# Kernel optimization log

Measured on AMD Instinct MI355X. Metric: run time of the kernel, lower is better.

Reference implementation:

```python
import jax, jax.numpy as jnp
import numpy as np

N, IN, HID, OUT, HD = 512, 256, 256, 256, 64  # n_agents, in_dim, hid_dim, out_dim, head_dim (out_dim // n_heads)


def _mlp2(x, w1, b1, w2, b2):
    return jax.nn.relu(x @ w1.T + b1) @ w2.T + b2


def setup_inputs():
    key = jax.random.key(0)
    ks = jax.random.split(key, 32)
    p = lambda i, shape: jax.random.normal(ks[i], shape, dtype=jnp.float32) * 0.05
    V = jax.random.normal(ks[0], (N, IN), dtype=jnp.float32)
    adj = jax.random.randint(ks[1], (N, N), 0, 2, dtype=jnp.int32)
    adj = adj.at[jnp.arange(N), jnp.arange(N)].set(1)  # self-loops so no softmax row is all -inf
    prev_hidden = jax.random.normal(ks[2], (N, HID), dtype=jnp.float32)
    return {
        "V": V, "adj": adj, "prev_hidden": prev_hidden,
        "W1": p(3, (HID, IN)), "sa0": p(4, (HID,)), "sa1": p(5, (HID,)),
        "ce_w1": p(6, (HID, 2 * IN)), "ce_b1": p(7, (HID,)), "ce_w2": p(8, (HD, HID)), "ce_b2": p(9, (HD,)),
        "ca0": p(10, (HD,)), "ca1": p(11, (HD,)),
        "te_w1": p(12, (HID, IN + HID)), "te_b1": p(13, (HID,)), "te_w2": p(14, (HD, HID)), "te_b2": p(15, (HD,)),
        "ta0": p(16, (HD,)), "ta1": p(17, (HD,)),
        "pe_w1": p(18, (HID, 3 * IN)), "pe_b1": p(19, (HID,)), "pe_w2": p(20, (HD, HID)), "pe_b2": p(21, (HD,)),
        "pa0": p(22, (HD,)), "pa1": p(23, (HD,)),
        "W2": p(24, (OUT, HID + 2 * HD + 1)), "op_w": p(25, (OUT, OUT)), "op_b": p(26, (OUT,)),
        "ln_g": jnp.ones((OUT,), jnp.float32), "ln_b": jnp.zeros((OUT,), jnp.float32),
    }


def _forward(V, adj, prev_hidden, W1, sa0, sa1, ce_w1, ce_b1, ce_w2, ce_b2, ca0, ca1,
             te_w1, te_b1, te_w2, te_b2, ta0, ta1, pe_w1, pe_b1, pe_w2, pe_b2, pa0, pa1,
             W2, op_w, op_b, ln_g, ln_b):
    neg = -jnp.inf
    # --- branch 1: standard GAT attention ---
    Wh1 = V @ W1.T                                             # (N, HID)
    s1 = (Wh1 @ sa0)[:, None] + (Wh1 @ sa1)[None, :]           # (N, N)
    s1 = jnp.where(adj == 0, neg, s1)
    H1 = jax.nn.softmax(s1, axis=1) @ Wh1                      # (N, HID)
    # --- branch 2: causal, all ordered pairs i != j ---
    wA, wB = ce_w1[:, :IN], ce_w1[:, IN:]
    h = jax.nn.relu((V @ wA.T)[:, None, :] + (V @ wB.T)[None, :, :] + ce_b1)  # (N, N, HID)
    f = h @ ce_w2.T + ce_b2                                    # (N, N, HD)
    s2 = jnp.where(jnp.eye(N, dtype=bool), neg, f @ (ca0 + ca1))
    a2 = jax.nn.softmax(s2.reshape(-1)).reshape(N, N)          # softmax over all off-diagonal pairs
    H2 = jnp.broadcast_to(jnp.einsum('ij,ijd->d', a2, f), (N, HD))
    # --- branch 3: temporal; (N,1) scores broadcast against (N,N) causal mask ---
    tf = _mlp2(jnp.concatenate([V, prev_hidden], -1), te_w1, te_b1, te_w2, te_b2)  # (N, HD)
    ts = tf @ (ta0 + ta1)                                      # (N,)
    cmask = jnp.triu(jnp.ones((N, N), dtype=bool), 1)
    s3 = jnp.where(cmask, neg, jnp.broadcast_to(ts[:, None], (N, N)))
    H3 = jax.nn.softmax(s3, axis=1) @ tf                       # (N, HD) == prefix means of tf
    # --- branch 4: cooperative; first two neighbors in index order (zeros if < 2) ---
    pos = jnp.where(adj == 1, jnp.arange(N)[None, :], N)
    srt = jnp.sort(pos, axis=1)
    i0, i1 = srt[:, 0], srt[:, 1]
    valid = (i1 < N)[:, None]
    n0 = jnp.where(valid, V[jnp.clip(i0, 0, N - 1)], 0.0)
    n1 = jnp.where(valid, V[jnp.clip(i1, 0, N - 1)], 0.0)
    cf = _mlp2(jnp.concatenate([V, n0, n1], -1), pe_w1, pe_b1, pe_w2, pe_b2)  # (N, HD)
    # torch: softmax over dim of size 1 -> all ones, alpha^T @ cf == column sums -> (HD,)
    # then unsqueezed to (HD,1) and zero-padded to (N,1) since HD < N  (faithful to source bug)
    H4v = cf.sum(axis=0)
    H4 = jnp.concatenate([H4v, jnp.zeros((N - HD,), V.dtype)])[:, None]       # (N, 1)
    # --- combine ---
    Hc = jnp.concatenate([H1, H2, H3, H4], axis=-1) @ W2.T     # (N, OUT)
    out = Hc @ op_w.T + op_b
    mu = out.mean(-1, keepdims=True)
    var = ((out - mu) ** 2).mean(-1, keepdims=True)
    y = (out - mu) / jnp.sqrt(var + 1e-5) * ln_g + ln_b        # LayerNorm, eps=1e-5
    return jax.nn.elu(y)                                       # dropout is identity in eval


def reference(V, adj, prev_hidden, W1, sa0, sa1, ce_w1, ce_b1, ce_w2, ce_b2, ca0, ca1,
              te_w1, te_b1, te_w2, te_b2, ta0, ta1, pe_w1, pe_b1, pe_w2, pe_b2, pa0, pa1,
              W2, op_w, op_b, ln_g, ln_b):
    return _forward(V, adj, prev_hidden, W1, sa0, sa1, ce_w1, ce_b1, ce_w2, ce_b2, ca0, ca1,
                    te_w1, te_b1, te_w2, te_b2, ta0, ta1, pe_w1, pe_b1, pe_w2, pe_b2, pa0, pa1,
                    W2, op_w, op_b, ln_g, ln_b)
```

## Files before the change

### kernel.cpp

```cpp
#include <hip/hip_runtime.h>

typedef unsigned short u16;

constexpr int kN   = 512;
constexpr int kIN  = 256;
constexpr int kHID = 256;
constexpr int kHD  = 64;
constexpr int kOUT = 256;

__device__ __forceinline__ float us2f(u16 u){
  union { unsigned int i; float f; } c; c.i = ((unsigned int)u) << 16; return c.f;
}
__device__ __forceinline__ u16 f2us(float f){
  union { float f; unsigned int i; } c; c.f = f;
  unsigned int r = c.i + 0x7fff + ((c.i >> 16) & 1);
  return (u16)(r >> 16);
}

__device__ bool probe_is_f32(const unsigned int* __restrict__ V){
  __shared__ int cnt;
  if (threadIdx.x == 0) cnt = 0;
  __syncthreads();
  int c = 0;
  for (int k = threadIdx.x; k < 4096; k += 256){
    float x = us2f((u16)(V[k] & 0xffffu));
    if (!(fabsf(x) <= 32.0f)) c++;
  }
  atomicAdd(&cnt, c);
  __syncthreads();
  return cnt > 64;
}

struct ConvArgs { const void* src[23]; float* dst[23]; int n[23]; };

__global__ __launch_bounds__(256) void k_conv(ConvArgs a, const unsigned int* __restrict__ Vraw,
                                              const int* __restrict__ adj, int* __restrict__ flag,
                                              float* __restrict__ Xp, float* __restrict__ e1v)
{
  int b = blockIdx.x, tid = threadIdx.x;
  bool f32 = probe_is_f32(Vraw);
  if (b < 256){
    if (b == 0){
      if (tid == 0) *flag = f32 ? 1 : 0;
      e1v[tid] = 0.f; e1v[tid + 256] = 0.f;
    }
    int t = b*256 + tid;
    const int stride = 65536;
    for (int s = 0; s < 23; ++s){
      int n4 = a.n[s] >> 2;
      float4* d = (float4*)a.dst[s];
      if (f32){
        const float4* sf = (const float4*)a.src[s];
        for (int i = t; i < n4; i += stride) d[i] = sf[i];
      } else {
        const ushort4* sb = (const ushort4*)a.src[s];
        for (int i = t; i < n4; i += stride){
          ushort4 u = sb[i];
          d[i] = make_float4(us2f(u.x), us2f(u.y), us2f(u.z), us2f(u.w));
        }
      }
    }
  } else {
    __shared__ unsigned long long msk[8];
    __shared__ int sj[2];
    int i = b - 256;
    int w = tid >> 6, lane = tid & 63;
    unsigned long long m0 = __ballot(adj[(size_t)i*kN + tid] != 0);
    unsigned long long m1 = __ballot(adj[(size_t)i*kN + 256 + tid] != 0);
    if (lane == 0){ msk[w] = m0; msk[4 + w] = m1; }
    __syncthreads();
    if (tid == 0){
      int j0 = -1, j1 = -1;
      for (int c = 0; c < 8 && j1 < 0; ++c){
        unsigned long long m = msk[c];
        while (m && j1 < 0){
          int bb = __builtin_ctzll(m);
          int j = c*64 + bb;
          if (j0 < 0) j0 = j; else j1 = j;
          m &= m - 1;
        }
      }
      if (j1 < 0) j0 = -1;
      sj[0] = j0; sj[1] = j1;
    }
    __syncthreads();
    int j0 = sj[0], j1 = sj[1];
    const float* Vf = (const float*)Vraw;
    const u16*  Vb = (const u16*)Vraw;
    auto rdV = [&](int r, int k)->float{
      return f32 ? Vf[(size_t)r*kIN + k] : us2f(Vb[(size_t)r*kIN + k]);
    };
    Xp[(size_t)i*768 + tid]       = rdV(i, tid);
    Xp[(size_t)i*768 + 256 + tid] = (j0 >= 0) ? rdV(j0, tid) : 0.f;
    Xp[(size_t)i*768 + 512 + tid] = (j1 >= 0) ? rdV(j1, tid) : 0.f;
  }
}

__device__ __forceinline__ float blk_red(float v, float* tmp, bool isMax){
  int lane = threadIdx.x & 63, wv = threadIdx.x >> 6;
  #pragma unroll
  for (int o = 32; o > 0; o >>= 1){
    float t = __shfl_down(v, o, 64);
    v = isMax ? fmaxf(v, t) : (v + t);
  }
  __syncthreads();
  if (lane == 0) tmp[wv] = v;
  __syncthreads();
  float r = tmp[0];
  for (int i = 1; i < 4; ++i) r = isMax ? fmaxf(r, tmp[i]) : (r + tmp[i]);
  return r;
}

struct WSP {
  const int* adj; const int* flag; void* out;
  float *Vf,*prevf,*W1f,*sa1f,*cw1f,*cb1f,*cw2f,*cb2f,*ca0f,*ca1f;
  float *tw1f,*tb1f,*tw2f,*tb2f,*pw1f,*pb1f,*pw2f,*pb2f;
  float *W2f,*opwf,*opbf,*lngf,*lnbf;
  float *tw2t,*pw2t,*Wcomb,*OM,*ow4;
  float *Wh1,*e1v,*wadj,*Hc,*Am,*Bm,*uvec,*beta;
  float *s2,*maxp,*zp,*MZ,*gsum;
  float *htp0,*htp1,*hpp0,*hpp1,*hpp2,*hidden_t,*hidden_p;
  float *tfm,*cfm,*H4v,*Xp,*out3;
};

struct GSeg2 { const float* X; const float* W; float* C; int ldx, ldw, ldc, K; };
struct GArgs2 { GSeg2 s[8]; const float* sa1; float* e1; };

__global__ __launch_bounds__(256) void k_gemmA(GArgs2 ga)
{
  __shared__ __align__(16) float Xs[2][32][68];
  __shared__ __align__(16) float Ws[2][32][68];
  const GSeg2 sg = ga.s[blockIdx.y];
  const int tm = blockIdx.x & 7;
  const int tn = blockIdx.x >> 3;
  const int i0 = tm << 6;
  const int n0 = tn << 6;
  const int tid = threadIdx.x;

  const int xrow = tid >> 3;
  const int xk   = (tid & 7) << 2;
  const int rg = (tid >> 4) << 2;
  const int cg = (tid & 15) << 2;

  const float* Xb = sg.X + (size_t)i0 * sg.ldx;
  const float* Wb = sg.W + (size_t)n0 * sg.ldw;

  float4 xr0, xr1, wr0, wr1;
  auto loadT = [&](int kt){
    xr0 = *(const float4*)(Xb + (size_t)xrow * sg.ldx + kt + xk);
    xr1 = *(const float4*)(Xb + (size_t)(xrow+32) * sg.ldx + kt + xk);
    wr0 = *(const float4*)(Wb + (size_t)xrow * sg.ldw + kt + xk);
    wr1 = *(const float4*)(Wb + (size_t)(xrow+32) * sg.ldw + kt + xk);
  };
  auto writeT = [&](int bu){
    Xs[bu][xk+0][xrow] = xr0.x;  Xs[bu][xk+1][xrow] = xr0.y;
    Xs[bu][xk+2][xrow] = xr0.z;  Xs[bu][xk+3][xrow] = xr0.w;
    Xs[bu][xk+0][xrow+32] = xr1.x;  Xs[bu][xk+1][xrow+32] = xr1.y;
    Xs[bu][xk+2][xrow+32] = xr1.z;  Xs[bu][xk+3][xrow+32] = xr1.w;
    Ws[bu][xk+0][xrow]    = wr0.x; Ws[bu][xk+1][xrow]    = wr0.y;
    Ws[bu][xk+2][xrow]    = wr0.z; Ws[bu][xk+3][xrow]    = wr0.w;
    Ws[bu][xk+0][xrow+32] = wr1.x; Ws[bu][xk+1][xrow+32] = wr1.y;
    Ws[bu][xk+2][xrow+32] = wr1.z; Ws[bu][xk+3][xrow+32] = wr1.w;
  };

  loadT(0); writeT(0); __syncthreads();

  float acc[4][4] = {};
  const int nkt = sg.K >> 5;
  for (int t = 0; t < nkt; ++t){
    if (t + 1 < nkt) loadT((t + 1) << 5);
    const int bu = t & 1;
    #pragma unroll
    for (int kk = 0; kk < 32; ++kk){
      const float4 av = *(const float4*)&Xs[bu][kk][rg];
      const float4 bv = *(const float4*)&Ws[bu][kk][cg];
      acc[0][0]+=av.x*bv.x; acc[0][1]+=av.x*bv.y; acc[0][2]+=av.x*bv.z; acc[0][3]+=av.x*bv.w;
      acc[1][0]+=av.y*bv.x; acc[1][1]+=av.y*bv.y; acc[1][2]+=av.y*bv.z; acc[1][3]+=av.y*bv.w;
      acc[2][0]+=av.z*bv.x; acc[2][1]+=av.z*bv.y; acc[2][2]+=av.z*bv.z; acc[2][3]+=av.z*bv.w;
      acc[3][0]+=av.w*bv.x; acc[3][1]+=av.w*bv.y; acc[3][2]+=av.w*bv.z; acc[3][3]+=av.w*bv.w;
    }
    if (t + 1 < nkt) writeT((t + 1) & 1);
    __syncthreads();
  }

  #pragma unroll
  for (int ri = 0; ri < 4; ++ri)
    *(float4*)(sg.C + (size_t)(i0 + rg + ri) * sg.ldc + (n0 + cg)) =
      make_float4(acc[ri][0], acc[ri][1], acc[ri][2], acc[ri][3]);

  if (blockIdx.y == 0){
    int cb = n0 + cg;
    float s0 = ga.sa1[cb], s1 = ga.sa1[cb+1], s2v = ga.sa1[cb+2], s3 = ga.sa1[cb+3];
    #pragma unroll
    for (int ri = 0; ri < 4; ++ri){
      float v = acc[ri][0]*s0 + acc[ri][1]*s1 + acc[ri][2]*s2v + acc[ri][3]*s3;
      v += __shfl_xor(v, 1, 16);
      v += __shfl_xor(v, 2, 16);
      v += __shfl_xor(v, 4, 16);
      v += __shfl_xor(v, 8, 16);
      if ((tid & 15) == 0) atomicAdd(&ga.e1[i0 + rg + ri], v);
    }
  }
}

struct GS32 { const float* X; const float* W; float* C; int ldx, ldw, ldc, K; int bkn; };

__device__ __forceinline__ void gemm32_body(const GS32 sg, int tm, int tn, int tid,
                                            float* Xs, float* Ws)
{
  const int i0 = tm << 5, n0 = tn << 5;
  const int xrow = tid >> 3;
  const int xk = (tid & 7) << 2;
  const int rg = (tid >> 4) << 1;
  const int cg = (tid & 15) << 1;
  const float* Xb = sg.X + (size_t)i0 * sg.ldx;
  const float* Wb = sg.bkn ? (sg.W + n0) : (sg.W + (size_t)n0 * sg.ldw);
  float4 xr, wr;
  auto loadT = [&](int kt){
    xr = *(const float4*)(Xb + (size_t)xrow * sg.ldx + kt + xk);
    if (sg.bkn) wr = *(const float4*)(Wb + (size_t)(kt + xrow) * sg.ldw + xk);
    else        wr = *(const float4*)(Wb + (size_t)xrow * sg.ldw + kt + xk);
  };
  auto writeT = [&](int bu){
    float* xs = Xs + bu*1152;
    xs[(xk+0)*36 + xrow] = xr.x; xs[(xk+1)*36 + xrow] = xr.y;
    xs[(xk+2)*36 + xrow] = xr.z; xs[(xk+3)*36 + xrow] = xr.w;
    float* wsp = Ws + bu*1152;
    if (sg.bkn){
      wsp[xrow*36 + xk+0] = wr.x; wsp[xrow*36 + xk+1] = wr.y;
      wsp[xrow*36 + xk+2] = wr.z; wsp[xrow*36 + xk+3] = wr.w;
    } else {
      wsp[(xk+0)*36 + xrow] = wr.x; wsp[(xk+1)*36 + xrow] = wr.y;
      wsp[(xk+2)*36 + xrow] = wr.z; wsp[(xk+3)*36 + xrow] = wr.w;
    }
  };
  loadT(0); writeT(0); __syncthreads();
  float a00=0,a01=0,a10=0,a11=0;
  const int nkt = sg.K >> 5;
  for (int t = 0; t < nkt; ++t){
    if (t+1 < nkt) loadT((t+1) << 5);
    const float* xs = Xs + (t&1)*1152;
    const float* wsp = Ws + (t&1)*1152;
    #pragma unroll
    for (int kk = 0; kk < 32; ++kk){
      float2 av = *(const float2*)&xs[kk*36 + rg];
      float2 bv = *(const float2*)&wsp[kk*36 + cg];
      a00 += av.x*bv.x; a01 += av.x*bv.y;
      a10 += av.y*bv.x; a11 += av.y*bv.y;
    }
    if (t+1 < nkt) writeT((t+1)&1);
    __syncthreads();
  }
  float* cp = sg.C + (size_t)(i0+rg)*sg.ldc + n0 + cg;
  *(float2*)cp = make_float2(a00, a01);
  *(float2*)(cp + sg.ldc) = make_float2(a10, a11);
}

__global__ __launch_bounds__(256) void k_stage2(WSP w)
{
  __shared__ __align__(16) char smem[18432];
  float* st = (float*)smem;
  int b = blockIdx.x, tid = threadIdx.x;
  if (b < 128){
    int f = b*256 + tid;
    int c4 = f & 63;
    {
      float4 a = ((const float4*)w.htp0)[f], bb = ((const float4*)w.htp1)[f];
      float4 bi = ((const float4*)w.tb1f)[c4];
      ((float4*)w.hidden_t)[f] = make_float4(
        fmaxf(a.x+bb.x+bi.x,0.f), fmaxf(a.y+bb.y+bi.y,0.f),
        fmaxf(a.z+bb.z+bi.z,0.f), fmaxf(a.w+bb.w+bi.w,0.f));
    }
    {
      float4 a = ((const float4*)w.hpp0)[f], bb = ((const float4*)w.hpp1)[f];
      float4 c = ((const float4*)w.hpp2)[f];
      float4 bi = ((const float4*)w.pb1f)[c4];
      ((float4*)w.hidden_p)[f] = make_float4(
        fmaxf(a.x+bb.x+c.x+bi.x,0.f), fmaxf(a.y+bb.y+c.y+bi.y,0.f),
        fmaxf(a.z+bb.z+c.z+bi.z,0.f), fmaxf(a.w+bb.w+c.w+bi.w,0.f));
    }
  } else if (b < 640){
    int i = b - 128;
    int m0 = w.adj[(size_t)i*kN + tid];
    int m1 = w.adj[(size_t)i*kN + tid + 256];
    float ea = w.e1v[tid], eb = w.e1v[tid+256];
    float v0 = m0 ? ea : -1e30f;
    float v1 = m1 ? eb : -1e30f;
    float m = blk_red(fmaxf(v0, v1), st, true);
    float z = blk_red((m0 ? expf(ea-m) : 0.f) + (m1 ? expf(eb-m) : 0.f), st, false);
    float iz = 1.0f / z;
    w.wadj[(size_t)i*kN + tid]       = m0 ? expf(ea - m) * iz : 0.f;
    w.wadj[(size_t)i*kN + tid + 256] = m1 ? expf(eb - m) * iz : 0.f;
  } else if (b == 640){
    if (tid < 64){ st[tid] = w.ca0f[tid] + w.ca1f[tid]; w.H4v[tid] = 0.f; }
    __syncthreads();
    float a = 0.f;
    for (int d = 0; d < kHD; ++d) a += w.cw2f[(size_t)d*kHID + tid] * st[d];
    w.uvec[tid] = a;
    if (tid == 0){
      float bsum = 0.f;
      for (int d = 0; d < kHD; ++d) bsum += w.cb2f[d] * st[d];
      *w.beta = bsum;
    }
  } else if (b < 643){
    const float* src = (b == 641) ? w.tw2f : w.pw2f;
    float* dst = (b == 641) ? w.tw2t : w.pw2t;
    for (int ch = 0; ch < 4; ++ch){
      __syncthreads();
      #pragma unroll
      for (int e = 0; e < 16; ++e){
        int lin = e*256 + tid;
        int r = lin >> 6, c = lin & 63;
        st[r*65 + c] = src[(size_t)r*256 + ch*64 + c];
      }
      __syncthreads();
      #pragma unroll
      for (int e = 0; e < 16; ++e){
        int lin = e*256 + tid;
        int kc = lin >> 6, dd = lin & 63;
        dst[(size_t)(ch*64 + kc)*64 + dd] = st[dd*65 + kc];
      }
    }
  } else if (b < 723){
    int q = b - 643;
    int tm = q & 7, tn = q >> 3;
    const float* Wsrc = w.W2f + ((tn < 8) ? 0 : 64);
    GS32 sg{w.opwf, Wsrc, w.Wcomb, 256, 385, 320, 256, 1};
    gemm32_body(sg, tm, tn, tid, (float*)smem, (float*)(smem + 9216));
  } else if (b < 739){
    int q = b - 723;
    GS32 sg{w.opwf, w.W2f + 256, w.OM, 256, 385, 64, 256, 1};
    gemm32_body(sg, q & 7, q >> 3, tid, (float*)smem, (float*)(smem + 9216));
  } else {
    st[tid] = w.W2f[(size_t)tid*385 + 384];
    __syncthreads();
    float a = 0.f;
    const float* orow = w.opwf + (size_t)tid*256;
    for (int m = 0; m < 256; m += 4){
      float4 o4 = *(const float4*)(orow + m);
      a += o4.x*st[m] + o4.y*st[m+1] + o4.z*st[m+2] + o4.w*st[m+3];
    }
    w.ow4[tid] = a;
  }
}

__global__ __launch_bounds__(256) void k_stage3(WSP w)
{
  __shared__ __align__(16) float smem3[4*256 + 256];
  int b = blockIdx.x, tid = threadIdx.x;
  if (b < 64){
    int m = b >> 5, grp = b & 31;
    const float* X  = m ? w.hidden_p : w.hidden_t;
    const float* Wt = m ? w.pw2t : w.tw2t;
    const float* bi = m ? w.pb2f : w.tb2f;
    float* C = m ? w.cfm : w.tfm;
    int i0 = grp*16 + (tid >> 6)*4;
    int d = tid & 63;
    const float* x0 = X + (size_t)i0*256;
    const float* x1 = x0 + 256;
    const float* x2 = x0 + 512;
    const float* x3 = x0 + 768;
    float a0=0.f, a1=0.f, a2=0.f, a3=0.f;
    for (int k = 0; k < 256; k += 4){
      float w0 = Wt[(size_t)(k+0)*64 + d];
      float w1 = Wt[(size_t)(k+1)*64 + d];
      float w2 = Wt[(size_t)(k+2)*64 + d];
      float w3 = Wt[(size_t)(k+3)*64 + d];
      float4 f0 = *(const float4*)(x0 + k);
      float4 f1 = *(const float4*)(x1 + k);
      float4 f2 = *(const float4*)(x2 + k);
      float4 f3 = *(const float4*)(x3 + k);
      a0 += f0.x*w0 + f0.y*w1 + f0.z*w2 + f0.w*w3;
      a1 += f1.x*w0 + f1.y*w1 + f1.z*w2 + f1.w*w3;
      a2 += f2.x*w0 + f2.y*w1 + f2.z*w2 + f2.w*w3;
      a3 += f3.x*w0 + f3.y*w1 + f3.z*w2 + f3.w*w3;
    }
    float bd = bi[d];
    C[(size_t)(i0+0)*64 + d] = a0 + bd;
    C[(size_t)(i0+1)*64 + d] = a1 + bd;
    C[(size_t)(i0+2)*64 + d] = a2 + bd;
    C[(size_t)(i0+3)*64 + d] = a3 + bd;
  } else {
    float* aib = smem3;
    float* uu  = smem3 + 1024;
    int q = b - 64;
    int i0 = (q & 127) * 4, j0 = (q >> 7) * 64;
    int wv = tid >> 6, lane = tid & 63;
    uu[tid] = w.uvec[tid];
    float b1v = w.cb1f[tid];
    #pragma unroll
    for (int r = 0; r < 4; ++r) aib[r*256 + tid] = w.Am[(size_t)(i0+r)*kHID + tid] + b1v;
    __syncthreads();
    int i = i0 + wv, j = j0 + lane;
    const float4* bp = (const float4*)(w.Bm + (size_t)j*kHID);
    float acc = *w.beta;
    #pragma unroll 8
    for (int k4 = 0; k4 < kHID/4; ++k4){
      float4 bv = bp[k4];
      float4 a4 = *(const float4*)&aib[wv*256 + k4*4];
      float4 u4 = *(const float4*)&uu[k4*4];
      acc += fmaxf(a4.x+bv.x,0.f)*u4.x + fmaxf(a4.y+bv.y,0.f)*u4.y
           + fmaxf(a4.z+bv.z,0.f)*u4.z + fmaxf(a4.w+bv.w,0.f)*u4.w;
    }
    if (j == i) acc = -1e30f;
    w.s2[(size_t)i*kN + j] = acc;
    float m = acc;
    #pragma unroll
    for (int o = 32; o > 0; o >>= 1) m = fmaxf(m, __shfl_down(m, o, 64));
    m = __shfl(m, 0, 64);
    float e = expf(acc - m);
    #pragma unroll
    for (int o = 32; o > 0; o >>= 1) e += __shfl_down(e, o, 64);
    if (lane == 0){
      int pb = q*4 + wv;
      w.maxp[pb] = m; w.zp[pb] = e;
    }
  }
}

__global__ __launch_bounds__(256) void k_stage4(WSP w)
{
  __shared__ __align__(16) char smem[18432];
  int b = blockIdx.x, tid = threadIdx.x;
  if (b < 128){
    GS32 sg{w.wadj, w.Wh1, w.Hc, 512, 256, 320, 512, 1};
    gemm32_body(sg, b & 15, b >> 4, tid, (float*)smem, (float*)(smem + 9216));
  } else if (b < 192){
    int d = b - 128;
    int lane = tid & 63, wv = tid >> 6;
    float v0 = w.tfm[(size_t)(2*tid)*kHD + d];
    float v1 = w.tfm[(size_t)(2*tid+1)*kHD + d];
    float s = v0 + v1;
    float x = s;
    #pragma unroll
    for (int off = 1; off < 64; off <<= 1){
      float y = __shfl_up(x, off, 64);
      if (lane >= off) x += y;
    }
    float* wsum = (float*)smem;
    if (lane == 63) wsum[wv] = x;
    __syncthreads();
    float base = 0.f;
    for (int k = 0; k < wv; ++k) base += wsum[k];
    float excl = base + x - s;
    w.Hc[(size_t)(2*tid)*320 + 256 + d]   = (excl + v0) / (float)(2*tid + 1);
    w.Hc[(size_t)(2*tid+1)*320 + 256 + d] = (excl + s)  / (float)(2*tid + 2);
  } else if (b < 200){
    float* sm = (float*)smem;
    int d = tid & 63, sub = tid >> 6;
    int r0 = (b-192)*64 + sub*16;
    float s = 0.f;
    #pragma unroll
    for (int e = 0; e < 16; ++e) s += w.cfm[(size_t)(r0+e)*kHD + d];
    sm[sub*64 + d] = s;
    __syncthreads();
    if (tid < 64)
      atomicAdd(&w.H4v[tid], sm[tid] + sm[64+tid] + sm[128+tid] + sm[192+tid]);
  } else {
    float* red = (float*)smem;
    float m = -1e30f;
    #pragma unroll
    for (int r = 0; r < 16; ++r) m = fmaxf(m, w.maxp[tid + 256*r]);
    m = blk_red(m, red, true);
    float z = 0.f;
    #pragma unroll
    for (int r = 0; r < 16; ++r) z += w.zp[tid + 256*r] * expf(w.maxp[tid + 256*r] - m);
    z = blk_red(z, red, false);
    if (tid == 0){ w.MZ[0] = m; w.MZ[1] = z; }
    w.gsum[tid] = 0.f;
  }
}

__global__ __launch_bounds__(256) void k_stage5(WSP w)
{
  __shared__ __align__(16) char smem[18432];
  int b = blockIdx.x, tid = threadIdx.x;
  if (b < 1024){
    float* wt = (float*)smem;
    int i0 = (b & 31) * 16, j0 = (b >> 5) * 16;
    float M = w.MZ[0], invZ = 1.0f / w.MZ[1];
    {
      int r = tid >> 4, c = tid & 15;
      wt[r*16 + c] = expf(w.s2[(size_t)(i0+r)*kN + (j0+c)] - M) * invZ;
    }
    float b1v = w.cb1f[tid];
    float aib[16];
    #pragma unroll
    for (int r = 0; r < 16; ++r) aib[r] = w.Am[(size_t)(i0+r)*kHID + tid] + b1v;
    __syncthreads();
    float acc = 0.f;
    for (int j = 0; j < 16; ++j){
      float bj = w.Bm[(size_t)(j0+j)*kHID + tid];
      #pragma unroll
      for (int r = 0; r < 16; ++r)
        acc += wt[r*16 + j] * fmaxf(aib[r] + bj, 0.f);
    }
    atomicAdd(&w.gsum[tid], acc);
  } else {
    int q = b - 1024;
    GS32 sg{w.Hc, w.Wcomb, w.out3, 320, 320, 256, 320, 0};
    gemm32_body(sg, q & 15, q >> 4, tid, (float*)smem, (float*)(smem + 9216));
  }
}

__global__ __launch_bounds__(256) void k_final(WSP w)
{
  __shared__ float gs[kHID];
  __shared__ float part[kHD][4];
  __shared__ float h2s[kHD];
  __shared__ float cc2s[kOUT];
  int b = blockIdx.x, tid = threadIdx.x;
  gs[tid] = w.gsum[tid];
  __syncthreads();
  {
    int dd = tid >> 2, q = tid & 3;
    float a = 0.f;
    for (int kk = 0; kk < 64; ++kk){
      int k = q*64 + kk;
      a += gs[k] * w.cw2f[(size_t)dd*kHID + k];
    }
    part[dd][q] = a;
  }
  __syncthreads();
  if (tid < kHD)
    h2s[tid] = w.cb2f[tid] + part[tid][0] + part[tid][1] + part[tid][2] + part[tid][3];
  __syncthreads();
  {
    float a = 0.f;
    const float* om = w.OM + (size_t)tid*64;
    for (int d = 0; d < kHD; d += 4){
      float4 o4 = *(const float4*)(om + d);
      a += o4.x*h2s[d] + o4.y*h2s[d+1] + o4.z*h2s[d+2] + o4.w*h2s[d+3];
    }
    cc2s[tid] = a;
  }
  __syncthreads();
  int row = b*4 + (tid >> 6), lane = tid & 63;
  float h4r = (row < kHD) ? w.H4v[row] : 0.f;
  float4 v  = *(const float4*)(w.out3 + (size_t)row*kOUT + lane*4);
  float4 c2 = *(const float4*)(&cc2s[lane*4]);
  float4 o4 = *(const float4*)(w.ow4 + lane*4);
  float4 pb = *(const float4*)(w.opbf + lane*4);
  v.x += c2.x + h4r*o4.x + pb.x;
  v.y += c2.y + h4r*o4.y + pb.y;
  v.z += c2.z + h4r*o4.z + pb.z;
  v.w += c2.w + h4r*o4.w + pb.w;
  float s = v.x + v.y + v.z + v.w;
  #pragma unroll
  for (int o = 32; o > 0; o >>= 1) s += __shfl_xor(s, o, 64);
  float mu = s * (1.0f/kOUT);
  float dx = v.x-mu, dy = v.y-mu, dz = v.z-mu, dw = v.w-mu;
  float ss = dx*dx + dy*dy + dz*dz + dw*dw;
  #pragma unroll
  for (int o = 32; o > 0; o >>= 1) ss += __shfl_xor(ss, o, 64);
  float rs = rsqrtf(ss * (1.0f/kOUT) + 1e-5f);
  float4 g  = *(const float4*)(w.lngf + lane*4);
  float4 be = *(const float4*)(w.lnbf + lane*4);
  float y0 = dx*rs*g.x + be.x, y1 = dy*rs*g.y + be.y;
  float y2 = dz*rs*g.z + be.z, y3 = dw*rs*g.w + be.w;
  y0 = (y0 > 0.f) ? y0 : expm1f(y0);
  y1 = (y1 > 0.f) ? y1 : expm1f(y1);
  y2 = (y2 > 0.f) ? y2 : expm1f(y2);
  y3 = (y3 > 0.f) ? y3 : expm1f(y3);
  if (*w.flag){
    *(float4*)((float*)w.out + (size_t)row*kOUT + lane*4) = make_float4(y0,y1,y2,y3);
  } else {
    ushort4 u; u.x = f2us(y0); u.y = f2us(y1); u.z = f2us(y2); u.w = f2us(y3);
    ((ushort4*)w.out)[(size_t)row*64 + lane] = u;
  }
}

extern "C" void kernel_launch(void* const* d_in, const int* in_sizes, int n_in,
                              void* d_out, int out_size, void* d_ws, size_t ws_size,
                              hipStream_t stream)
{
  const void* V     = d_in[0];
  const int*  adj   = (const int*)d_in[1];
  const void* prev  = d_in[2];
  const void* W1    = d_in[3];
  const void* sa1   = d_in[5];
  const void* ce_w1 = d_in[6];
  const void* ce_b1 = d_in[7];
  const void* ce_w2 = d_in[8];
  const void* ce_b2 = d_in[9];
  const void* ca0   = d_in[10];
  const void* ca1   = d_in[11];
  const void* te_w1 = d_in[12];
  const void* te_b1 = d_in[13];
  const void* te_w2 = d_in[14];
  const void* te_b2 = d_in[15];
  const void* pe_w1 = d_in[18];
  const void* pe_b1 = d_in[19];
  const void* pe_w2 = d_in[20];
  const void* pe_b2 = d_in[21];
  const void* W2    = d_in[24];
  const void* op_w  = d_in[25];
  const void* op_b  = d_in[26];
  const void* ln_g  = d_in[27];
  const void* ln_b  = d_in[28];

  float* ws  = (float*)d_ws;
  int*  flag = (int*)ws;
  float* p   = ws + 16;
  float* Vf   = p; p += 131072;
  float* prevf= p; p += 131072;
  float* W1f  = p; p += 65536;
  float* sa1f = p; p += 256;
  float* cw1f = p; p += 131072;
  float* cb1f = p; p += 256;
  float* cw2f = p; p += 16384;
  float* cb2f = p; p += 64;
  float* ca0f = p; p += 64;
  float* ca1f = p; p += 64;
  float* tw1f = p; p += 131072;
  float* tb1f = p; p += 256;
  float* tw2f = p; p += 16384;
  float* tb2f = p; p += 64;
  float* pw1f = p; p += 196608;
  float* pb1f = p; p += 256;
  float* pw2f = p; p += 16384;
  float* pb2f = p; p += 64;
  float* W2f  = p; p += 98560;
  float* opwf = p; p += 65536;
  float* opbf = p; p += 256;
  float* lngf = p; p += 256;
  float* lnbf = p; p += 256;
  float* tw2t = p; p += 16384;
  float* pw2t = p; p += 16384;
  float* Wcomb= p; p += 81920;
  float* OM   = p; p += 16384;
  float* ow4  = p; p += 256;
  float* Wh1      = p; p += 131072;
  float* e1v      = p; p += 512;
  float* wadj     = p; p += 262144;
  float* Hc       = p; p += 163840;
  float* Am       = p; p += 131072;
  float* Bm       = p; p += 131072;
  float* uvec     = p; p += 256;
  float* beta     = p; p += 16;
  float* s2       = p; p += 262144;
  float* maxp     = p; p += 4096;
  float* zpart    = p; p += 4096;
  float* MZ       = p; p += 16;
  float* gsum     = p; p += 256;
  float* htp0     = p; p += 131072;
  float* htp1     = p; p += 131072;
  float* hpp0     = p; p += 131072;
  float* hpp1     = p; p += 131072;
  float* hpp2     = p; p += 131072;
  float* hidden_t = p; p += 131072;
  float* hidden_p = p; p += 131072;
  float* tfm      = p; p += 32768;
  float* cfm      = p; p += 32768;
  float* H4v      = p; p += 64;
  float* Xp       = p; p += 393216;
  float* out3     = p; p += 131072;

  WSP w;
  w.adj = adj; w.flag = flag; w.out = d_out;
  w.Vf=Vf; w.prevf=prevf; w.W1f=W1f; w.sa1f=sa1f; w.cw1f=cw1f; w.cb1f=cb1f;
  w.cw2f=cw2f; w.cb2f=cb2f; w.ca0f=ca0f; w.ca1f=ca1f;
  w.tw1f=tw1f; w.tb1f=tb1f; w.tw2f=tw2f; w.tb2f=tb2f;
  w.pw1f=pw1f; w.pb1f=pb1f; w.pw2f=pw2f; w.pb2f=pb2f;
  w.W2f=W2f; w.opwf=opwf; w.opbf=opbf; w.lngf=lngf; w.lnbf=lnbf;
  w.tw2t=tw2t; w.pw2t=pw2t; w.Wcomb=Wcomb; w.OM=OM; w.ow4=ow4;
  w.Wh1=Wh1; w.e1v=e1v; w.wadj=wadj; w.Hc=Hc;
  w.Am=Am; w.Bm=Bm; w.uvec=uvec; w.beta=beta;
  w.s2=s2; w.maxp=maxp; w.zp=zpart; w.MZ=MZ; w.gsum=gsum;
  w.htp0=htp0; w.htp1=htp1; w.hpp0=hpp0; w.hpp1=hpp1; w.hpp2=hpp2;
  w.hidden_t=hidden_t; w.hidden_p=hidden_p;
  w.tfm=tfm; w.cfm=cfm; w.H4v=H4v; w.Xp=Xp; w.out3=out3;

  {
    ConvArgs ca;
    const void* srcs[23] = {V, prev, W1, sa1, ce_w1, ce_b1, ce_w2, ce_b2, ca0, ca1,
                            te_w1, te_b1, te_w2, te_b2, pe_w1, pe_b1, pe_w2, pe_b2,
                            W2, op_w, op_b, ln_g, ln_b};
    float* dsts[23] = {Vf, prevf, W1f, sa1f, cw1f, cb1f, cw2f, cb2f, ca0f, ca1f,
                       tw1f, tb1f, tw2f, tb2f, pw1f, pb1f, pw2f, pb2f,
                       W2f, opwf, opbf, lngf, lnbf};
    int ns[23] = {131072, 131072, 65536, 256, 131072, 256, 16384, 64, 64, 64,
                  131072, 256, 16384, 64, 196608, 256, 16384, 64,
                  98560, 65536, 256, 256, 256};
    for (int s = 0; s < 23; ++s){ ca.src[s] = srcs[s]; ca.dst[s] = dsts[s]; ca.n[s] = ns[s]; }
    k_conv<<<768, 256, 0, stream>>>(ca, (const unsigned int*)V, adj, flag, Xp, e1v);
  }

  {
    GArgs2 g{};
    g.s[0] = {Vf,       W1f,        Wh1,  256, 256, 256, 256};
    g.s[1] = {Vf,       cw1f,       Am,   256, 512, 256, 256};
    g.s[2] = {Vf,       cw1f + 256, Bm,   256, 512, 256, 256};
    g.s[3] = {Vf,       tw1f,       htp0, 256, 512, 256, 256};
    g.s[4] = {prevf,    tw1f + 256, htp1, 256, 512, 256, 256};
    g.s[5] = {Xp,       pw1f,       hpp0, 768, 768, 256, 256};
    g.s[6] = {Xp + 256, pw1f + 256, hpp1, 768, 768, 256, 256};
    g.s[7] = {Xp + 512, pw1f + 512, hpp2, 768, 768, 256, 256};
    g.sa1 = sa1f; g.e1 = e1v;
    k_gemmA<<<dim3(32, 8), 256, 0, stream>>>(g);
  }

  k_stage2<<<740, 256, 0, stream>>>(w);

  k_stage3<<<1088, 256, 0, stream>>>(w);

  k_stage4<<<201, 256, 0, stream>>>(w);

  k_stage5<<<1152, 256, 0, stream>>>(w);

  k_final<<<128, 256, 0, stream>>>(w);
}
```

Before: 243.0 us.

## Fuse all stages into one cooperative persistent kernel with grid syncs

Replaces seven separate kernel launches with a single cooperative persistent kernel that loops over stages and separates them with grid-wide barriers. Stage work is repacked, so some independent pieces (weight transposes, the uvec/beta reduction, the W2/op_w combination GEMMs) move earlier and read raw inputs directly. The goal is to remove launch gaps and tail effects between stages. In exchange it adds grid.sync cost, a larger per-block shared-memory footprint that may limit occupancy, and a fallback path of per-stage launches.

```diff
diff --git a/kernel.cpp b/kernel.cpp
--- a/kernel.cpp
+++ b/kernel.cpp
@@ -1,4 +1,7 @@
 #include <hip/hip_runtime.h>
+#include <hip/hip_cooperative_groups.h>
+
+namespace cg = cooperative_groups;
 
 typedef unsigned short u16;
 
@@ -15,6 +18,9 @@
   union { float f; unsigned int i; } c; c.f = f;
   unsigned int r = c.i + 0x7fff + ((c.i >> 16) & 1);
   return (u16)(r >> 16);
+}
+__device__ __forceinline__ float ldraw(const void* p, size_t i, bool f32){
+  return f32 ? ((const float*)p)[i] : us2f(((const u16*)p)[i]);
 }
 
 __device__ bool probe_is_f32(const unsigned int* __restrict__ V){
@@ -31,71 +37,6 @@
   return cnt > 64;
 }
 
-struct ConvArgs { const void* src[23]; float* dst[23]; int n[23]; };
-
-__global__ __launch_bounds__(256) void k_conv(ConvArgs a, const unsigned int* __restrict__ Vraw,
-                                              const int* __restrict__ adj, int* __restrict__ flag,
-                                              float* __restrict__ Xp, float* __restrict__ e1v)
-{
-  int b = blockIdx.x, tid = threadIdx.x;
-  bool f32 = probe_is_f32(Vraw);
-  if (b < 256){
-    if (b == 0){
-      if (tid == 0) *flag = f32 ? 1 : 0;
-      e1v[tid] = 0.f; e1v[tid + 256] = 0.f;
-    }
-    int t = b*256 + tid;
-    const int stride = 65536;
-    for (int s = 0; s < 23; ++s){
-      int n4 = a.n[s] >> 2;
-      float4* d = (float4*)a.dst[s];
-      if (f32){
-        const float4* sf = (const float4*)a.src[s];
-        for (int i = t; i < n4; i += stride) d[i] = sf[i];
-      } else {
-        const ushort4* sb = (const ushort4*)a.src[s];
-        for (int i = t; i < n4; i += stride){
-          ushort4 u = sb[i];
-          d[i] = make_float4(us2f(u.x), us2f(u.y), us2f(u.z), us2f(u.w));
-        }
-      }
-    }
-  } else {
-    __shared__ unsigned long long msk[8];
-    __shared__ int sj[2];
-    int i = b - 256;
-    int w = tid >> 6, lane = tid & 63;
-    unsigned long long m0 = __ballot(adj[(size_t)i*kN + tid] != 0);
-    unsigned long long m1 = __ballot(adj[(size_t)i*kN + 256 + tid] != 0);
-    if (lane == 0){ msk[w] = m0; msk[4 + w] = m1; }
-    __syncthreads();
-    if (tid == 0){
-      int j0 = -1, j1 = -1;
-      for (int c = 0; c < 8 && j1 < 0; ++c){
-        unsigned long long m = msk[c];
-        while (m && j1 < 0){
-          int bb = __builtin_ctzll(m);
-          int j = c*64 + bb;
-          if (j0 < 0) j0 = j; else j1 = j;
-          m &= m - 1;
-        }
-      }
-      if (j1 < 0) j0 = -1;
-      sj[0] = j0; sj[1] = j1;
-    }
-    __syncthreads();
-    int j0 = sj[0], j1 = sj[1];
-    const float* Vf = (const float*)Vraw;
-    const u16*  Vb = (const u16*)Vraw;
-    auto rdV = [&](int r, int k)->float{
-      return f32 ? Vf[(size_t)r*kIN + k] : us2f(Vb[(size_t)r*kIN + k]);
-    };
-    Xp[(size_t)i*768 + tid]       = rdV(i, tid);
-    Xp[(size_t)i*768 + 256 + tid] = (j0 >= 0) ? rdV(j0, tid) : 0.f;
-    Xp[(size_t)i*768 + 512 + tid] = (j1 >= 0) ? rdV(j1, tid) : 0.f;
-  }
-}
-
 __device__ __forceinline__ float blk_red(float v, float* tmp, bool isMax){
   int lane = threadIdx.x & 63, wv = threadIdx.x >> 6;
   #pragma unroll
@@ -111,8 +52,15 @@
   return r;
 }
 
-struct WSP {
-  const int* adj; const int* flag; void* out;
+struct ConvArgs { const void* src[23]; float* dst[23]; int n[23]; };
+struct GSeg2 { const float* X; const float* W; float* C; int ldx, ldw, ldc, K; };
+struct GS32 { const float* X; const float* W; float* C; int ldx, ldw, ldc, K; int bkn; };
+
+struct MegaArgs {
+  const unsigned int* Vraw;
+  const int* adj;
+  int* flag; void* out;
+  const void *rca0,*rca1,*rcw2,*rcb2,*rtw2,*rpw2;
   float *Vf,*prevf,*W1f,*sa1f,*cw1f,*cb1f,*cw2f,*cb2f,*ca0f,*ca1f;
   float *tw1f,*tb1f,*tw2f,*tb2f,*pw1f,*pb1f,*pw2f,*pb2f;
   float *W2f,*opwf,*opbf,*lngf,*lnbf;
@@ -121,89 +69,9 @@
   float *s2,*maxp,*zp,*MZ,*gsum;
   float *htp0,*htp1,*hpp0,*hpp1,*hpp2,*hidden_t,*hidden_p;
   float *tfm,*cfm,*H4v,*Xp,*out3;
+  ConvArgs ca;
+  GSeg2 gs[8];
 };
-
-struct GSeg2 { const float* X; const float* W; float* C; int ldx, ldw, ldc, K; };
-struct GArgs2 { GSeg2 s[8]; const float* sa1; float* e1; };
-
-__global__ __launch_bounds__(256) void k_gemmA(GArgs2 ga)
-{
-  __shared__ __align__(16) float Xs[2][32][68];
-  __shared__ __align__(16) float Ws[2][32][68];
-  const GSeg2 sg = ga.s[blockIdx.y];
-  const int tm = blockIdx.x & 7;
-  const int tn = blockIdx.x >> 3;
-  const int i0 = tm << 6;
-  const int n0 = tn << 6;
-  const int tid = threadIdx.x;
-
-  const int xrow = tid >> 3;
-  const int xk   = (tid & 7) << 2;
-  const int rg = (tid >> 4) << 2;
-  const int cg = (tid & 15) << 2;
-
-  const float* Xb = sg.X + (size_t)i0 * sg.ldx;
-  const float* Wb = sg.W + (size_t)n0 * sg.ldw;
-
-  float4 xr0, xr1, wr0, wr1;
-  auto loadT = [&](int kt){
-    xr0 = *(const float4*)(Xb + (size_t)xrow * sg.ldx + kt + xk);
-    xr1 = *(const float4*)(Xb + (size_t)(xrow+32) * sg.ldx + kt + xk);
-    wr0 = *(const float4*)(Wb + (size_t)xrow * sg.ldw + kt + xk);
-    wr1 = *(const float4*)(Wb + (size_t)(xrow+32) * sg.ldw + kt + xk);
-  };
-  auto writeT = [&](int bu){
-    Xs[bu][xk+0][xrow] = xr0.x;  Xs[bu][xk+1][xrow] = xr0.y;
-    Xs[bu][xk+2][xrow] = xr0.z;  Xs[bu][xk+3][xrow] = xr0.w;
-    Xs[bu][xk+0][xrow+32] = xr1.x;  Xs[bu][xk+1][xrow+32] = xr1.y;
-    Xs[bu][xk+2][xrow+32] = xr1.z;  Xs[bu][xk+3][xrow+32] = xr1.w;
-    Ws[bu][xk+0][xrow]    = wr0.x; Ws[bu][xk+1][xrow]    = wr0.y;
-    Ws[bu][xk+2][xrow]    = wr0.z; Ws[bu][xk+3][xrow]    = wr0.w;
-    Ws[bu][xk+0][xrow+32] = wr1.x; Ws[bu][xk+1][xrow+32] = wr1.y;
-    Ws[bu][xk+2][xrow+32] = wr1.z; Ws[bu][xk+3][xrow+32] = wr1.w;
-  };
-
-  loadT(0); writeT(0); __syncthreads();
-
-  float acc[4][4] = {};
-  const int nkt = sg.K >> 5;
-  for (int t = 0; t < nkt; ++t){
-    if (t + 1 < nkt) loadT((t + 1) << 5);
-    const int bu = t & 1;
-    #pragma unroll
-    for (int kk = 0; kk < 32; ++kk){
-      const float4 av = *(const float4*)&Xs[bu][kk][rg];
-      const float4 bv = *(const float4*)&Ws[bu][kk][cg];
-      acc[0][0]+=av.x*bv.x; acc[0][1]+=av.x*bv.y; acc[0][2]+=av.x*bv.z; acc[0][3]+=av.x*bv.w;
-      acc[1][0]+=av.y*bv.x; acc[1][1]+=av.y*bv.y; acc[1][2]+=av.y*bv.z; acc[1][3]+=av.y*bv.w;
-      acc[2][0]+=av.z*bv.x; acc[2][1]+=av.z*bv.y; acc[2][2]+=av.z*bv.z; acc[2][3]+=av.z*bv.w;
-      acc[3][0]+=av.w*bv.x; acc[3][1]+=av.w*bv.y; acc[3][2]+=av.w*bv.z; acc[3][3]+=av.w*bv.w;
-    }
-    if (t + 1 < nkt) writeT((t + 1) & 1);
-    __syncthreads();
-  }
-
-  #pragma unroll
-  for (int ri = 0; ri < 4; ++ri)
-    *(float4*)(sg.C + (size_t)(i0 + rg + ri) * sg.ldc + (n0 + cg)) =
-      make_float4(acc[ri][0], acc[ri][1], acc[ri][2], acc[ri][3]);
-
-  if (blockIdx.y == 0){
-    int cb = n0 + cg;
-    float s0 = ga.sa1[cb], s1 = ga.sa1[cb+1], s2v = ga.sa1[cb+2], s3 = ga.sa1[cb+3];
-    #pragma unroll
-    for (int ri = 0; ri < 4; ++ri){
-      float v = acc[ri][0]*s0 + acc[ri][1]*s1 + acc[ri][2]*s2v + acc[ri][3]*s3;
-      v += __shfl_xor(v, 1, 16);
-      v += __shfl_xor(v, 2, 16);
-      v += __shfl_xor(v, 4, 16);
-      v += __shfl_xor(v, 8, 16);
-      if ((tid & 15) == 0) atomicAdd(&ga.e1[i0 + rg + ri], v);
-    }
-  }
-}
-
-struct GS32 { const float* X; const float* W; float* C; int ldx, ldw, ldc, K; int bkn; };
 
 __device__ __forceinline__ void gemm32_body(const GS32 sg, int tm, int tn, int tid,
                                             float* Xs, float* Ws)
@@ -256,104 +124,236 @@
   *(float2*)(cp + sg.ldc) = make_float2(a10, a11);
 }
 
-__global__ __launch_bounds__(256) void k_stage2(WSP w)
-{
-  __shared__ __align__(16) char smem[18432];
-  float* st = (float*)smem;
-  int b = blockIdx.x, tid = threadIdx.x;
-  if (b < 128){
-    int f = b*256 + tid;
+
+__device__ void body_s0(const MegaArgs& A, int it, int tid, bool f32, char* SM)
+{
+  if (it < 256){
+    if (it == 0){
+      if (tid == 0) *A.flag = f32 ? 1 : 0;
+      A.e1v[tid] = 0.f; A.e1v[tid + 256] = 0.f;
+    }
+    int t = it*256 + tid;
+    for (int s = 0; s < 23; ++s){
+      int n4 = A.ca.n[s] >> 2;
+      float4* d = (float4*)A.ca.dst[s];
+      if (f32){
+        const float4* sf = (const float4*)A.ca.src[s];
+        for (int i = t; i < n4; i += 65536) d[i] = sf[i];
+      } else {
+        const ushort4* sb = (const ushort4*)A.ca.src[s];
+        for (int i = t; i < n4; i += 65536){
+          ushort4 u = sb[i];
+          d[i] = make_float4(us2f(u.x), us2f(u.y), us2f(u.z), us2f(u.w));
+        }
+      }
+    }
+  } else if (it < 768){
+    unsigned long long* msk = (unsigned long long*)SM;
+    int* sj = (int*)(SM + 64);
+    int i = it - 256;
+    int w = tid >> 6, lane = tid & 63;
+    unsigned long long m0 = __ballot(A.adj[(size_t)i*kN + tid] != 0);
+    unsigned long long m1 = __ballot(A.adj[(size_t)i*kN + 256 + tid] != 0);
+    if (lane == 0){ msk[w] = m0; msk[4 + w] = m1; }
+    __syncthreads();
+    if (tid == 0){
+      int j0 = -1, j1 = -1;
+      for (int c = 0; c < 8 && j1 < 0; ++c){
+        unsigned long long m = msk[c];
+        while (m && j1 < 0){
+          int bb = __builtin_ctzll(m);
+          int j = c*64 + bb;
+          if (j0 < 0) j0 = j; else j1 = j;
+          m &= m - 1;
+        }
+      }
+      if (j1 < 0) j0 = -1;
+      sj[0] = j0; sj[1] = j1;
+    }
+    __syncthreads();
+    int j0 = sj[0], j1 = sj[1];
+    A.Xp[(size_t)i*768 + tid]       = ldraw(A.Vraw, (size_t)i*kIN + tid, f32);
+    A.Xp[(size_t)i*768 + 256 + tid] = (j0 >= 0) ? ldraw(A.Vraw, (size_t)j0*kIN + tid, f32) : 0.f;
+    A.Xp[(size_t)i*768 + 512 + tid] = (j1 >= 0) ? ldraw(A.Vraw, (size_t)j1*kIN + tid, f32) : 0.f;
+  } else if (it == 768){
+    float* st = (float*)SM;
+    if (tid < 64){ st[tid] = ldraw(A.rca0, tid, f32) + ldraw(A.rca1, tid, f32); A.H4v[tid] = 0.f; }
+    __syncthreads();
+    float a = 0.f;
+    for (int d = 0; d < kHD; ++d) a += ldraw(A.rcw2, (size_t)d*kHID + tid, f32) * st[d];
+    A.uvec[tid] = a;
+    if (tid == 0){
+      float b = 0.f;
+      for (int d = 0; d < kHD; ++d) b += ldraw(A.rcb2, d, f32) * st[d];
+      *A.beta = b;
+    }
+  } else {
+    const void* src = (it == 769) ? A.rtw2 : A.rpw2;
+    float* dst = (it == 769) ? A.tw2t : A.pw2t;
+    float* st = (float*)SM;
+    for (int ch = 0; ch < 4; ++ch){
+      __syncthreads();
+      #pragma unroll
+      for (int e = 0; e < 16; ++e){
+        int lin = e*256 + tid, r = lin >> 6, c = lin & 63;
+        st[r*65 + c] = ldraw(src, (size_t)r*256 + ch*64 + c, f32);
+      }
+      __syncthreads();
+      #pragma unroll
+      for (int e = 0; e < 16; ++e){
+        int lin = e*256 + tid, kc = lin >> 6, dd = lin & 63;
+        dst[(size_t)(ch*64 + kc)*64 + dd] = st[dd*65 + kc];
+      }
+    }
+  }
+}
+
+__device__ void body_gemmA(const MegaArgs& A, int it, int tid, char* SM)
+{
+  float (*Xs)[32][68] = (float (*)[32][68])SM;
+  float (*Ws)[32][68] = (float (*)[32][68])(SM + 17408);
+  int seg = it >> 5, x = it & 31;
+  const GSeg2 sg = A.gs[seg];
+  const int tm = x & 7, tn = x >> 3;
+  const int i0 = tm << 6, n0 = tn << 6;
+
+  const int xrow = tid >> 3;
+  const int xk   = (tid & 7) << 2;
+  const int rg = (tid >> 4) << 2;
+  const int cg = (tid & 15) << 2;
+
+  const float* Xb = sg.X + (size_t)i0 * sg.ldx;
+  const float* Wb = sg.W + (size_t)n0 * sg.ldw;
+
+  float4 xr0, xr1, wr0, wr1;
+  auto loadT = [&](int kt){
+    xr0 = *(const float4*)(Xb + (size_t)xrow * sg.ldx + kt + xk);
+    xr1 = *(const float4*)(Xb + (size_t)(xrow+32) * sg.ldx + kt + xk);
+    wr0 = *(const float4*)(Wb + (size_t)xrow * sg.ldw + kt + xk);
+    wr1 = *(const float4*)(Wb + (size_t)(xrow+32) * sg.ldw + kt + xk);
+  };
+  auto writeT = [&](int bu){
+    Xs[bu][xk+0][xrow] = xr0.x;  Xs[bu][xk+1][xrow] = xr0.y;
+    Xs[bu][xk+2][xrow] = xr0.z;  Xs[bu][xk+3][xrow] = xr0.w;
+    Xs[bu][xk+0][xrow+32] = xr1.x;  Xs[bu][xk+1][xrow+32] = xr1.y;
+    Xs[bu][xk+2][xrow+32] = xr1.z;  Xs[bu][xk+3][xrow+32] = xr1.w;
+    Ws[bu][xk+0][xrow]    = wr0.x; Ws[bu][xk+1][xrow]    = wr0.y;
+    Ws[bu][xk+2][xrow]    = wr0.z; Ws[bu][xk+3][xrow]    = wr0.w;
+    Ws[bu][xk+0][xrow+32] = wr1.x; Ws[bu][xk+1][xrow+32] = wr1.y;
+    Ws[bu][xk+2][xrow+32] = wr1.z; Ws[bu][xk+3][xrow+32] = wr1.w;
+  };
+
+  loadT(0); writeT(0); __syncthreads();
+
+  float acc[4][4] = {};
+  const int nkt = sg.K >> 5;
+  for (int t = 0; t < nkt; ++t){
+    if (t + 1 < nkt) loadT((t + 1) << 5);
+    const int bu = t & 1;
+    #pragma unroll
+    for (int kk = 0; kk < 32; ++kk){
+      const float4 av = *(const float4*)&Xs[bu][kk][rg];
+      const float4 bv = *(const float4*)&Ws[bu][kk][cg];
+      acc[0][0]+=av.x*bv.x; acc[0][1]+=av.x*bv.y; acc[0][2]+=av.x*bv.z; acc[0][3]+=av.x*bv.w;
+      acc[1][0]+=av.y*bv.x; acc[1][1]+=av.y*bv.y; acc[1][2]+=av.y*bv.z; acc[1][3]+=av.y*bv.w;
+      acc[2][0]+=av.z*bv.x; acc[2][1]+=av.z*bv.y; acc[2][2]+=av.z*bv.z; acc[2][3]+=av.z*bv.w;
+      acc[3][0]+=av.w*bv.x; acc[3][1]+=av.w*bv.y; acc[3][2]+=av.w*bv.z; acc[3][3]+=av.w*bv.w;
+    }
+    if (t + 1 < nkt) writeT((t + 1) & 1);
+    __syncthreads();
+  }
+
+  #pragma unroll
+  for (int ri = 0; ri < 4; ++ri)
+    *(float4*)(sg.C + (size_t)(i0 + rg + ri) * sg.ldc + (n0 + cg)) =
+      make_float4(acc[ri][0], acc[ri][1], acc[ri][2], acc[ri][3]);
+
+  if (seg == 0){
+    int cb = n0 + cg;
+    float s0 = A.sa1f[cb], s1 = A.sa1f[cb+1], s2v = A.sa1f[cb+2], s3 = A.sa1f[cb+3];
+    #pragma unroll
+    for (int ri = 0; ri < 4; ++ri){
+      float v = acc[ri][0]*s0 + acc[ri][1]*s1 + acc[ri][2]*s2v + acc[ri][3]*s3;
+      v += __shfl_xor(v, 1, 16);
+      v += __shfl_xor(v, 2, 16);
+      v += __shfl_xor(v, 4, 16);
+      v += __shfl_xor(v, 8, 16);
+      if ((tid & 15) == 0) atomicAdd(&A.e1v[i0 + rg + ri], v);
+    }
+  }
+}
+
+__device__ void body_s1(const MegaArgs& A, int it, int tid, char* SM)
+{
+  if (it < 256){
+    body_gemmA(A, it, tid, SM);
+  } else if (it < 336){
+    int q = it - 256, tm = q & 7, tn = q >> 3;
+    const float* Wsrc = A.W2f + ((tn < 8) ? 0 : 64);
+    GS32 sg{A.opwf, Wsrc, A.Wcomb, 256, 385, 320, 256, 1};
+    gemm32_body(sg, tm, tn, tid, (float*)SM, (float*)(SM + 9216));
+  } else if (it < 352){
+    int q = it - 336;
+    GS32 sg{A.opwf, A.W2f + 256, A.OM, 256, 385, 64, 256, 1};
+    gemm32_body(sg, q & 7, q >> 3, tid, (float*)SM, (float*)(SM + 9216));
+  } else {
+    float* st = (float*)SM;
+    st[tid] = A.W2f[(size_t)tid*385 + 384];
+    __syncthreads();
+    float a = 0.f;
+    const float* orow = A.opwf + (size_t)tid*256;
+    for (int m = 0; m < 256; m += 4){
+      float4 o4 = *(const float4*)(orow + m);
+      a += o4.x*st[m] + o4.y*st[m+1] + o4.z*st[m+2] + o4.w*st[m+3];
+    }
+    A.ow4[tid] = a;
+  }
+}
+
+__device__ void body_s2(const MegaArgs& A, int it, int tid, char* SM)
+{
+  if (it < 128){
+    int f = it*256 + tid;
     int c4 = f & 63;
     {
-      float4 a = ((const float4*)w.htp0)[f], bb = ((const float4*)w.htp1)[f];
-      float4 bi = ((const float4*)w.tb1f)[c4];
-      ((float4*)w.hidden_t)[f] = make_float4(
+      float4 a = ((const float4*)A.htp0)[f], bb = ((const float4*)A.htp1)[f];
+      float4 bi = ((const float4*)A.tb1f)[c4];
+      ((float4*)A.hidden_t)[f] = make_float4(
         fmaxf(a.x+bb.x+bi.x,0.f), fmaxf(a.y+bb.y+bi.y,0.f),
         fmaxf(a.z+bb.z+bi.z,0.f), fmaxf(a.w+bb.w+bi.w,0.f));
     }
     {
-      float4 a = ((const float4*)w.hpp0)[f], bb = ((const float4*)w.hpp1)[f];
-      float4 c = ((const float4*)w.hpp2)[f];
-      float4 bi = ((const float4*)w.pb1f)[c4];
-      ((float4*)w.hidden_p)[f] = make_float4(
+      float4 a = ((const float4*)A.hpp0)[f], bb = ((const float4*)A.hpp1)[f];
+      float4 c = ((const float4*)A.hpp2)[f];
+      float4 bi = ((const float4*)A.pb1f)[c4];
+      ((float4*)A.hidden_p)[f] = make_float4(
         fmaxf(a.x+bb.x+c.x+bi.x,0.f), fmaxf(a.y+bb.y+c.y+bi.y,0.f),
         fmaxf(a.z+bb.z+c.z+bi.z,0.f), fmaxf(a.w+bb.w+c.w+bi.w,0.f));
     }
-  } else if (b < 640){
-    int i = b - 128;
-    int m0 = w.adj[(size_t)i*kN + tid];
-    int m1 = w.adj[(size_t)i*kN + tid + 256];
-    float ea = w.e1v[tid], eb = w.e1v[tid+256];
+  } else {
+    float* st = (float*)SM;
+    int i = it - 128;
+    int m0 = A.adj[(size_t)i*kN + tid];
+    int m1 = A.adj[(size_t)i*kN + tid + 256];
+    float ea = A.e1v[tid], eb = A.e1v[tid+256];
     float v0 = m0 ? ea : -1e30f;
     float v1 = m1 ? eb : -1e30f;
     float m = blk_red(fmaxf(v0, v1), st, true);
     float z = blk_red((m0 ? expf(ea-m) : 0.f) + (m1 ? expf(eb-m) : 0.f), st, false);
     float iz = 1.0f / z;
-    w.wadj[(size_t)i*kN + tid]       = m0 ? expf(ea - m) * iz : 0.f;
-    w.wadj[(size_t)i*kN + tid + 256] = m1 ? expf(eb - m) * iz : 0.f;
-  } else if (b == 640){
-    if (tid < 64){ st[tid] = w.ca0f[tid] + w.ca1f[tid]; w.H4v[tid] = 0.f; }
-    __syncthreads();
-    float a = 0.f;
-    for (int d = 0; d < kHD; ++d) a += w.cw2f[(size_t)d*kHID + tid] * st[d];
-    w.uvec[tid] = a;
-    if (tid == 0){
-      float bsum = 0.f;
-      for (int d = 0; d < kHD; ++d) bsum += w.cb2f[d] * st[d];
-      *w.beta = bsum;
-    }
-  } else if (b < 643){
-    const float* src = (b == 641) ? w.tw2f : w.pw2f;
-    float* dst = (b == 641) ? w.tw2t : w.pw2t;
-    for (int ch = 0; ch < 4; ++ch){
-      __syncthreads();
-      #pragma unroll
-      for (int e = 0; e < 16; ++e){
-        int lin = e*256 + tid;
-        int r = lin >> 6, c = lin & 63;
-        st[r*65 + c] = src[(size_t)r*256 + ch*64 + c];
-      }
-      __syncthreads();
-      #pragma unroll
-      for (int e = 0; e < 16; ++e){
-        int lin = e*256 + tid;
-        int kc = lin >> 6, dd = lin & 63;
-        dst[(size_t)(ch*64 + kc)*64 + dd] = st[dd*65 + kc];
-      }
-    }
-  } else if (b < 723){
-    int q = b - 643;
-    int tm = q & 7, tn = q >> 3;
-    const float* Wsrc = w.W2f + ((tn < 8) ? 0 : 64);
-    GS32 sg{w.opwf, Wsrc, w.Wcomb, 256, 385, 320, 256, 1};
-    gemm32_body(sg, tm, tn, tid, (float*)smem, (float*)(smem + 9216));
-  } else if (b < 739){
-    int q = b - 723;
-    GS32 sg{w.opwf, w.W2f + 256, w.OM, 256, 385, 64, 256, 1};
-    gemm32_body(sg, q & 7, q >> 3, tid, (float*)smem, (float*)(smem + 9216));
-  } else {
-    st[tid] = w.W2f[(size_t)tid*385 + 384];
-    __syncthreads();
-    float a = 0.f;
-    const float* orow = w.opwf + (size_t)tid*256;
-    for (int m = 0; m < 256; m += 4){
-      float4 o4 = *(const float4*)(orow + m);
-      a += o4.x*st[m] + o4.y*st[m+1] + o4.z*st[m+2] + o4.w*st[m+3];
-    }
-    w.ow4[tid] = a;
-  }
-}
-
-__global__ __launch_bounds__(256) void k_stage3(WSP w)
-{
-  __shared__ __align__(16) float smem3[4*256 + 256];
-  int b = blockIdx.x, tid = threadIdx.x;
-  if (b < 64){
-    int m = b >> 5, grp = b & 31;
-    const float* X  = m ? w.hidden_p : w.hidden_t;
-    const float* Wt = m ? w.pw2t : w.tw2t;
-    const float* bi = m ? w.pb2f : w.tb2f;
-    float* C = m ? w.cfm : w.tfm;
+    A.wadj[(size_t)i*kN + tid]       = m0 ? expf(ea - m) * iz : 0.f;
+    A.wadj[(size_t)i*kN + tid + 256] = m1 ? expf(eb - m) * iz : 0.f;
+  }
+}
+
+__device__ void body_s3(const MegaArgs& A, int it, int tid, char* SM)
+{
+  if (it < 64){
+    int m = it >> 5, grp = it & 31;
+    const float* X  = m ? A.hidden_p : A.hidden_t;
+    const float* Wt = m ? A.pw2t : A.tw2t;
+    const float* bi = m ? A.pb2f : A.tb2f;
+    float* C = m ? A.cfm : A.tfm;
     int i0 = grp*16 + (tid >> 6)*4;
     int d = tid & 63;
     const float* x0 = X + (size_t)i0*256;
@@ -380,20 +380,20 @@
     C[(size_t)(i0+1)*64 + d] = a1 + bd;
     C[(size_t)(i0+2)*64 + d] = a2 + bd;
     C[(size_t)(i0+3)*64 + d] = a3 + bd;
-  } else {
-    float* aib = smem3;
-    float* uu  = smem3 + 1024;
-    int q = b - 64;
+  } else if (it < 1088){
+    float* aib = (float*)SM;
+    float* uu  = aib + 1024;
+    int q = it - 64;
     int i0 = (q & 127) * 4, j0 = (q >> 7) * 64;
     int wv = tid >> 6, lane = tid & 63;
-    uu[tid] = w.uvec[tid];
-    float b1v = w.cb1f[tid];
-    #pragma unroll
-    for (int r = 0; r < 4; ++r) aib[r*256 + tid] = w.Am[(size_t)(i0+r)*kHID + tid] + b1v;
+    uu[tid] = A.uvec[tid];
+    float b1v = A.cb1f[tid];
+    #pragma unroll
+    for (int r = 0; r < 4; ++r) aib[r*256 + tid] = A.Am[(size_t)(i0+r)*kHID + tid] + b1v;
     __syncthreads();
     int i = i0 + wv, j = j0 + lane;
-    const float4* bp = (const float4*)(w.Bm + (size_t)j*kHID);
-    float acc = *w.beta;
+    const float4* bp = (const float4*)(A.Bm + (size_t)j*kHID);
+    float acc = *A.beta;
     #pragma unroll 8
     for (int k4 = 0; k4 < kHID/4; ++k4){
       float4 bv = bp[k4];
@@ -403,7 +403,7 @@
            + fmaxf(a4.z+bv.z,0.f)*u4.z + fmaxf(a4.w+bv.w,0.f)*u4.w;
     }
     if (j == i) acc = -1e30f;
-    w.s2[(size_t)i*kN + j] = acc;
+    A.s2[(size_t)i*kN + j] = acc;
     float m = acc;
     #pragma unroll
     for (int o = 32; o > 0; o >>= 1) m = fmaxf(m, __shfl_down(m, o, 64));
@@ -413,23 +413,22 @@
     for (int o = 32; o > 0; o >>= 1) e += __shfl_down(e, o, 64);
     if (lane == 0){
       int pb = q*4 + wv;
-      w.maxp[pb] = m; w.zp[pb] = e;
-    }
-  }
-}
-
-__global__ __launch_bounds__(256) void k_stage4(WSP w)
-{
-  __shared__ __align__(16) char smem[18432];
-  int b = blockIdx.x, tid = threadIdx.x;
-  if (b < 128){
-    GS32 sg{w.wadj, w.Wh1, w.Hc, 512, 256, 320, 512, 1};
-    gemm32_body(sg, b & 15, b >> 4, tid, (float*)smem, (float*)(smem + 9216));
-  } else if (b < 192){
-    int d = b - 128;
+      A.maxp[pb] = m; A.zp[pb] = e;
+    }
+  } else {
+    int bb = it - 1088;
+    GS32 sg{A.wadj, A.Wh1, A.Hc, 512, 256, 320, 512, 1};
+    gemm32_body(sg, bb & 15, bb >> 4, tid, (float*)SM, (float*)(SM + 9216));
+  }
+}
+
+__device__ void body_s4(const MegaArgs& A, int it, int tid, char* SM)
+{
+  if (it < 64){
+    int d = it;
     int lane = tid & 63, wv = tid >> 6;
-    float v0 = w.tfm[(size_t)(2*tid)*kHD + d];
-    float v1 = w.tfm[(size_t)(2*tid+1)*kHD + d];
+    float v0 = A.tfm[(size_t)(2*tid)*kHD + d];
+    float v1 = A.tfm[(size_t)(2*tid+1)*kHD + d];
     float s = v0 + v1;
     float x = s;
     #pragma unroll
@@ -437,97 +436,94 @@
       float y = __shfl_up(x, off, 64);
       if (lane >= off) x += y;
     }
-    float* wsum = (float*)smem;
+    float* wsum = (float*)SM;
     if (lane == 63) wsum[wv] = x;
     __syncthreads();
     float base = 0.f;
     for (int k = 0; k < wv; ++k) base += wsum[k];
     float excl = base + x - s;
-    w.Hc[(size_t)(2*tid)*320 + 256 + d]   = (excl + v0) / (float)(2*tid + 1);
-    w.Hc[(size_t)(2*tid+1)*320 + 256 + d] = (excl + s)  / (float)(2*tid + 2);
-  } else if (b < 200){
-    float* sm = (float*)smem;
+    A.Hc[(size_t)(2*tid)*320 + 256 + d]   = (excl + v0) / (float)(2*tid + 1);
+    A.Hc[(size_t)(2*tid+1)*320 + 256 + d] = (excl + s)  / (float)(2*tid + 2);
+  } else if (it < 72){
+    float* sm = (float*)SM;
     int d = tid & 63, sub = tid >> 6;
-    int r0 = (b-192)*64 + sub*16;
+    int r0 = (it-64)*64 + sub*16;
     float s = 0.f;
     #pragma unroll
-    for (int e = 0; e < 16; ++e) s += w.cfm[(size_t)(r0+e)*kHD + d];
+    for (int e = 0; e < 16; ++e) s += A.cfm[(size_t)(r0+e)*kHD + d];
     sm[sub*64 + d] = s;
     __syncthreads();
     if (tid < 64)
-      atomicAdd(&w.H4v[tid], sm[tid] + sm[64+tid] + sm[128+tid] + sm[192+tid]);
+      atomicAdd(&A.H4v[tid], sm[tid] + sm[64+tid] + sm[128+tid] + sm[192+tid]);
   } else {
-    float* red = (float*)smem;
+    float* red = (float*)SM;
     float m = -1e30f;
     #pragma unroll
-    for (int r = 0; r < 16; ++r) m = fmaxf(m, w.maxp[tid + 256*r]);
+    for (int r = 0; r < 16; ++r) m = fmaxf(m, A.maxp[tid + 256*r]);
     m = blk_red(m, red, true);
     float z = 0.f;
     #pragma unroll
-    for (int r = 0; r < 16; ++r) z += w.zp[tid + 256*r] * expf(w.maxp[tid + 256*r] - m);
+    for (int r = 0; r < 16; ++r) z += A.zp[tid + 256*r] * expf(A.maxp[tid + 256*r] - m);
     z = blk_red(z, red, false);
-    if (tid == 0){ w.MZ[0] = m; w.MZ[1] = z; }
-    w.gsum[tid] = 0.f;
-  }
-}
-
-__global__ __launch_bounds__(256) void k_stage5(WSP w)
-{
-  __shared__ __align__(16) char smem[18432];
-  int b = blockIdx.x, tid = threadIdx.x;
-  if (b < 1024){
-    float* wt = (float*)smem;
-    int i0 = (b & 31) * 16, j0 = (b >> 5) * 16;
-    float M = w.MZ[0], invZ = 1.0f / w.MZ[1];
+    if (tid == 0){ A.MZ[0] = m; A.MZ[1] = z; }
+    A.gsum[tid] = 0.f;
+  }
+}
+
+__device__ void body_s5(const MegaArgs& A, int it, int tid, char* SM)
+{
+  if (it < 1024){
+    float* wt = (float*)SM;
+    int i0 = (it & 31) * 16, j0 = (it >> 5) * 16;
+    float M = A.MZ[0], invZ = 1.0f / A.MZ[1];
     {
       int r = tid >> 4, c = tid & 15;
-      wt[r*16 + c] = expf(w.s2[(size_t)(i0+r)*kN + (j0+c)] - M) * invZ;
-    }
-    float b1v = w.cb1f[tid];
+      wt[r*16 + c] = expf(A.s2[(size_t)(i0+r)*kN + (j0+c)] - M) * invZ;
+    }
+    float b1v = A.cb1f[tid];
     float aib[16];
     #pragma unroll
-    for (int r = 0; r < 16; ++r) aib[r] = w.Am[(size_t)(i0+r)*kHID + tid] + b1v;
+    for (int r = 0; r < 16; ++r) aib[r] = A.Am[(size_t)(i0+r)*kHID + tid] + b1v;
     __syncthreads();
     float acc = 0.f;
     for (int j = 0; j < 16; ++j){
-      float bj = w.Bm[(size_t)(j0+j)*kHID + tid];
+      float bj = A.Bm[(size_t)(j0+j)*kHID + tid];
       #pragma unroll
       for (int r = 0; r < 16; ++r)
         acc += wt[r*16 + j] * fmaxf(aib[r] + bj, 0.f);
     }
-    atomicAdd(&w.gsum[tid], acc);
+    atomicAdd(&A.gsum[tid], acc);
   } else {
-    int q = b - 1024;
-    GS32 sg{w.Hc, w.Wcomb, w.out3, 320, 320, 256, 320, 0};
-    gemm32_body(sg, q & 15, q >> 4, tid, (float*)smem, (float*)(smem + 9216));
-  }
-}
-
-__global__ __launch_bounds__(256) void k_final(WSP w)
-{
-  __shared__ float gs[kHID];
-  __shared__ float part[kHD][4];
-  __shared__ float h2s[kHD];
-  __shared__ float cc2s[kOUT];
-  int b = blockIdx.x, tid = threadIdx.x;
-  gs[tid] = w.gsum[tid];
+    int q = it - 1024;
+    GS32 sg{A.Hc, A.Wcomb, A.out3, 320, 320, 256, 320, 0};
+    gemm32_body(sg, q & 15, q >> 4, tid, (float*)SM, (float*)(SM + 9216));
+  }
+}
+
+__device__ void body_s6(const MegaArgs& A, int it, int tid, bool f32, char* SM)
+{
+  float* gs   = (float*)SM;
+  float* part = gs + 256;
+  float* h2s  = part + 256;
+  float* cc2s = h2s + 64;
+  gs[tid] = A.gsum[tid];
   __syncthreads();
   {
     int dd = tid >> 2, q = tid & 3;
     float a = 0.f;
     for (int kk = 0; kk < 64; ++kk){
       int k = q*64 + kk;
-      a += gs[k] * w.cw2f[(size_t)dd*kHID + k];
-    }
-    part[dd][q] = a;
+      a += gs[k] * A.cw2f[(size_t)dd*kHID + k];
+    }
+    part[dd*4 + q] = a;
   }
   __syncthreads();
   if (tid < kHD)
-    h2s[tid] = w.cb2f[tid] + part[tid][0] + part[tid][1] + part[tid][2] + part[tid][3];
+    h2s[tid] = A.cb2f[tid] + part[tid*4] + part[tid*4+1] + part[tid*4+2] + part[tid*4+3];
   __syncthreads();
   {
     float a = 0.f;
-    const float* om = w.OM + (size_t)tid*64;
+    const float* om = A.OM + (size_t)tid*64;
     for (int d = 0; d < kHD; d += 4){
       float4 o4 = *(const float4*)(om + d);
       a += o4.x*h2s[d] + o4.y*h2s[d+1] + o4.z*h2s[d+2] + o4.w*h2s[d+3];
@@ -535,12 +531,12 @@
     cc2s[tid] = a;
   }
   __syncthreads();
-  int row = b*4 + (tid >> 6), lane = tid & 63;
-  float h4r = (row < kHD) ? w.H4v[row] : 0.f;
-  float4 v  = *(const float4*)(w.out3 + (size_t)row*kOUT + lane*4);
+  int row = it*4 + (tid >> 6), lane = tid & 63;
+  float h4r = (row < kHD) ? A.H4v[row] : 0.f;
+  float4 v  = *(const float4*)(A.out3 + (size_t)row*kOUT + lane*4);
   float4 c2 = *(const float4*)(&cc2s[lane*4]);
-  float4 o4 = *(const float4*)(w.ow4 + lane*4);
-  float4 pb = *(const float4*)(w.opbf + lane*4);
+  float4 o4 = *(const float4*)(A.ow4 + lane*4);
+  float4 pb = *(const float4*)(A.opbf + lane*4);
   v.x += c2.x + h4r*o4.x + pb.x;
   v.y += c2.y + h4r*o4.y + pb.y;
   v.z += c2.z + h4r*o4.z + pb.z;
@@ -554,20 +550,68 @@
   #pragma unroll
   for (int o = 32; o > 0; o >>= 1) ss += __shfl_xor(ss, o, 64);
   float rs = rsqrtf(ss * (1.0f/kOUT) + 1e-5f);
-  float4 g  = *(const float4*)(w.lngf + lane*4);
-  float4 be = *(const float4*)(w.lnbf + lane*4);
+  float4 g  = *(const float4*)(A.lngf + lane*4);
+  float4 be = *(const float4*)(A.lnbf + lane*4);
   float y0 = dx*rs*g.x + be.x, y1 = dy*rs*g.y + be.y;
   float y2 = dz*rs*g.z + be.z, y3 = dw*rs*g.w + be.w;
   y0 = (y0 > 0.f) ? y0 : expm1f(y0);
   y1 = (y1 > 0.f) ? y1 : expm1f(y1);
   y2 = (y2 > 0.f) ? y2 : expm1f(y2);
   y3 = (y3 > 0.f) ? y3 : expm1f(y3);
-  if (*w.flag){
-    *(float4*)((float*)w.out + (size_t)row*kOUT + lane*4) = make_float4(y0,y1,y2,y3);
+  if (f32){
+    *(float4*)((float*)A.out + (size_t)row*kOUT + lane*4) = make_float4(y0,y1,y2,y3);
   } else {
     ushort4 u; u.x = f2us(y0); u.y = f2us(y1); u.z = f2us(y2); u.w = f2us(y3);
-    ((ushort4*)w.out)[(size_t)row*64 + lane] = u;
-  }
+    ((ushort4*)A.out)[(size_t)row*64 + lane] = u;
+  }
+}
+
+__device__ __forceinline__ int stage_count(int s){
+  switch(s){
+    case 0: return 771;  case 1: return 353;  case 2: return 640;
+    case 3: return 1216; case 4: return 73;   case 5: return 1152;
+    default: return 128;
+  }
+}
+
+__device__ void run_stage(int s, const MegaArgs& A, bool f32, char* SM, int b0, int nb)
+{
+  const int n = stage_count(s);
+  const int tid = threadIdx.x;
+  for (int it = b0; it < n; it += nb){
+    switch(s){
+      case 0: body_s0(A, it, tid, f32, SM); break;
+      case 1: body_s1(A, it, tid, SM); break;
+      case 2: body_s2(A, it, tid, SM); break;
+      case 3: body_s3(A, it, tid, SM); break;
+      case 4: body_s4(A, it, tid, SM); break;
+      case 5: body_s5(A, it, tid, SM); break;
+      default: body_s6(A, it, tid, f32, SM); break;
+    }
+    __syncthreads();
+  }
+}
+
+__global__ __launch_bounds__(256) void k_mega(MegaArgs A)
+{
+  __shared__ __align__(16) char SM[34816];
+  cg::grid_group grid = cg::this_grid();
+  bool f32 = probe_is_f32(A.Vraw);
+  #pragma unroll 1
+  for (int s = 0; s < 7; ++s){
+    run_stage(s, A, f32, SM, blockIdx.x, gridDim.x);
+    if (s < 6){ __threadfence(); grid.sync(); }
+  }
+}
+
+constexpr int kStageSM[7] = {16896, 34816, 64, 18432, 1024, 18432, 3328};
+
+template<int S>
+__global__ __launch_bounds__(256) void k_stage_one(MegaArgs A)
+{
+  __shared__ __align__(16) char SM[kStageSM[S]];
+  bool f32 = (S == 0) ? probe_is_f32(A.Vraw) : (*A.flag != 0);
+  run_stage(S, A, f32, SM, blockIdx.x, gridDim.x);
 }
 
 extern "C" void kernel_launch(void* const* d_in, const int* in_sizes, int n_in,
@@ -656,23 +700,23 @@
   float* Xp       = p; p += 393216;
   float* out3     = p; p += 131072;
 
-  WSP w;
-  w.adj = adj; w.flag = flag; w.out = d_out;
-  w.Vf=Vf; w.prevf=prevf; w.W1f=W1f; w.sa1f=sa1f; w.cw1f=cw1f; w.cb1f=cb1f;
-  w.cw2f=cw2f; w.cb2f=cb2f; w.ca0f=ca0f; w.ca1f=ca1f;
-  w.tw1f=tw1f; w.tb1f=tb1f; w.tw2f=tw2f; w.tb2f=tb2f;
-  w.pw1f=pw1f; w.pb1f=pb1f; w.pw2f=pw2f; w.pb2f=pb2f;
-  w.W2f=W2f; w.opwf=opwf; w.opbf=opbf; w.lngf=lngf; w.lnbf=lnbf;
-  w.tw2t=tw2t; w.pw2t=pw2t; w.Wcomb=Wcomb; w.OM=OM; w.ow4=ow4;
-  w.Wh1=Wh1; w.e1v=e1v; w.wadj=wadj; w.Hc=Hc;
-  w.Am=Am; w.Bm=Bm; w.uvec=uvec; w.beta=beta;
-  w.s2=s2; w.maxp=maxp; w.zp=zpart; w.MZ=MZ; w.gsum=gsum;
-  w.htp0=htp0; w.htp1=htp1; w.hpp0=hpp0; w.hpp1=hpp1; w.hpp2=hpp2;
-  w.hidden_t=hidden_t; w.hidden_p=hidden_p;
-  w.tfm=tfm; w.cfm=cfm; w.H4v=H4v; w.Xp=Xp; w.out3=out3;
+  MegaArgs A;
+  A.Vraw = (const unsigned int*)V; A.adj = adj; A.flag = flag; A.out = d_out;
+  A.rca0 = ca0; A.rca1 = ca1; A.rcw2 = ce_w2; A.rcb2 = ce_b2; A.rtw2 = te_w2; A.rpw2 = pe_w2;
+  A.Vf=Vf; A.prevf=prevf; A.W1f=W1f; A.sa1f=sa1f; A.cw1f=cw1f; A.cb1f=cb1f;
+  A.cw2f=cw2f; A.cb2f=cb2f; A.ca0f=ca0f; A.ca1f=ca1f;
+  A.tw1f=tw1f; A.tb1f=tb1f; A.tw2f=tw2f; A.tb2f=tb2f;
+  A.pw1f=pw1f; A.pb1f=pb1f; A.pw2f=pw2f; A.pb2f=pb2f;
+  A.W2f=W2f; A.opwf=opwf; A.opbf=opbf; A.lngf=lngf; A.lnbf=lnbf;
+  A.tw2t=tw2t; A.pw2t=pw2t; A.Wcomb=Wcomb; A.OM=OM; A.ow4=ow4;
+  A.Wh1=Wh1; A.e1v=e1v; A.wadj=wadj; A.Hc=Hc;
+  A.Am=Am; A.Bm=Bm; A.uvec=uvec; A.beta=beta;
+  A.s2=s2; A.maxp=maxp; A.zp=zpart; A.MZ=MZ; A.gsum=gsum;
+  A.htp0=htp0; A.htp1=htp1; A.hpp0=hpp0; A.hpp1=hpp1; A.hpp2=hpp2;
+  A.hidden_t=hidden_t; A.hidden_p=hidden_p;
+  A.tfm=tfm; A.cfm=cfm; A.H4v=H4v; A.Xp=Xp; A.out3=out3;
 
   {
-    ConvArgs ca;
     const void* srcs[23] = {V, prev, W1, sa1, ce_w1, ce_b1, ce_w2, ce_b2, ca0, ca1,
                             te_w1, te_b1, te_w2, te_b2, pe_w1, pe_b1, pe_w2, pe_b2,
                             W2, op_w, op_b, ln_g, ln_b};
@@ -682,31 +726,39 @@
     int ns[23] = {131072, 131072, 65536, 256, 131072, 256, 16384, 64, 64, 64,
                   131072, 256, 16384, 64, 196608, 256, 16384, 64,
                   98560, 65536, 256, 256, 256};
-    for (int s = 0; s < 23; ++s){ ca.src[s] = srcs[s]; ca.dst[s] = dsts[s]; ca.n[s] = ns[s]; }
-    k_conv<<<768, 256, 0, stream>>>(ca, (const unsigned int*)V, adj, flag, Xp, e1v);
-  }
-
-  {
-    GArgs2 g{};
-    g.s[0] = {Vf,       W1f,        Wh1,  256, 256, 256, 256};
-    g.s[1] = {Vf,       cw1f,       Am,   256, 512, 256, 256};
-    g.s[2] = {Vf,       cw1f + 256, Bm,   256, 512, 256, 256};
-    g.s[3] = {Vf,       tw1f,       htp0, 256, 512, 256, 256};
-    g.s[4] = {prevf,    tw1f + 256, htp1, 256, 512, 256, 256};
-    g.s[5] = {Xp,       pw1f,       hpp0, 768, 768, 256, 256};
-    g.s[6] = {Xp + 256, pw1f + 256, hpp1, 768, 768, 256, 256};
-    g.s[7] = {Xp + 512, pw1f + 512, hpp2, 768, 768, 256, 256};
-    g.sa1 = sa1f; g.e1 = e1v;
-    k_gemmA<<<dim3(32, 8), 256, 0, stream>>>(g);
-  }
-
-  k_stage2<<<740, 256, 0, stream>>>(w);
-
-  k_stage3<<<1088, 256, 0, stream>>>(w);
-
-  k_stage4<<<201, 256, 0, stream>>>(w);
-
-  k_stage5<<<1152, 256, 0, stream>>>(w);
-
-  k_final<<<128, 256, 0, stream>>>(w);
-}
+    for (int s = 0; s < 23; ++s){ A.ca.src[s] = srcs[s]; A.ca.dst[s] = dsts[s]; A.ca.n[s] = ns[s]; }
+  }
+  A.gs[0] = {Vf,       W1f,        Wh1,  256, 256, 256, 256};
+  A.gs[1] = {Vf,       cw1f,       Am,   256, 512, 256, 256};
+  A.gs[2] = {Vf,       cw1f + 256, Bm,   256, 512, 256, 256};
+  A.gs[3] = {Vf,       tw1f,       htp0, 256, 512, 256, 256};
+  A.gs[4] = {prevf,    tw1f + 256, htp1, 256, 512, 256, 256};
+  A.gs[5] = {Xp,       pw1f,       hpp0, 768, 768, 256, 256};
+  A.gs[6] = {Xp + 256, pw1f + 256, hpp1, 768, 768, 256, 256};
+  A.gs[7] = {Xp + 512, pw1f + 512, hpp2, 768, 768, 256, 256};
+
+  bool done = false;
+  int perCU = 0;
+  if (hipOccupancyMaxActiveBlocksPerMultiprocessor(&perCU,
+        reinterpret_cast<const void*>(&k_mega), 256, 0) != hipSuccess)
+    perCU = 0;
+  if (perCU > 0){
+    long long grid = (long long)perCU * 256;
+    if (grid > 1216) grid = 1216;
+    if (grid >= 64){
+      void* prm[] = { (void*)&A };
+      done = (hipLaunchCooperativeKernel(reinterpret_cast<const void*>(&k_mega),
+                dim3((unsigned)grid), dim3(256), prm, 0, stream) == hipSuccess);
+    }
+  }
+
+  if (!done){
+    k_stage_one<0><<<771, 256, 0, stream>>>(A);
+    k_stage_one<1><<<353, 256, 0, stream>>>(A);
+    k_stage_one<2><<<640, 256, 0, stream>>>(A);
+    k_stage_one<3><<<1216, 256, 0, stream>>>(A);
+    k_stage_one<4><<<73, 256, 0, stream>>>(A);
+    k_stage_one<5><<<1152, 256, 0, stream>>>(A);
+    k_stage_one<6><<<128, 256, 0, stream>>>(A);
+  }
+}
```

After: 273.9 us. 12.7% more time.
